# Kernel tuning notes

Measured on AMD Instinct MI355X. Metric: run time of the kernel, lower is better.

## Reference

```python
import jax, jax.numpy as jnp
import numpy as np

WEIGHT = 1.0
BIN_SIZE = 1.0
MAX_MZ = 2000.0
NUM_BINS = int(MAX_MZ / BIN_SIZE)  # 2000
B, N = 8192, 256


def setup_inputs() -> dict:
    key = jax.random.key(0)
    k1, k2, k3, k4, k5 = jax.random.split(key, 5)
    return {
        "pred_mz": jax.random.uniform(k1, (B, N), dtype=jnp.float32),
        "pred_intensity": jax.random.uniform(k2, (B, N), dtype=jnp.float32),
        "target_mz": jax.random.uniform(k3, (B, N), dtype=jnp.float32),
        "target_intensity": jax.random.uniform(k4, (B, N), dtype=jnp.float32),
        "target_mask": jax.random.uniform(k5, (B, N), dtype=jnp.float32),
    }


def _bin_spectrum(mz, intensity):
    # mz is normalized to [0,1]; denormalize and bin. Batched scatter-add:
    # a single 2D indexed add replaces the per-sample scatter_add_ loop.
    bin_idx = jnp.clip((mz * MAX_MZ / BIN_SIZE).astype(jnp.int32), 0, NUM_BINS - 1)  # [B, N]
    bsz = mz.shape[0]
    binned = jnp.zeros((bsz, NUM_BINS), dtype=intensity.dtype)
    return binned.at[jnp.arange(bsz)[:, None], bin_idx].add(intensity)


def reference(pred_mz, pred_intensity, target_mz, target_intensity, target_mask):
    pred_binned = _bin_spectrum(pred_mz, pred_intensity)                    # [B, NUM_BINS]
    target_binned = _bin_spectrum(target_mz, target_intensity * target_mask)
    eps = 1e-8  # matches torch F.cosine_similarity default
    pn = jnp.maximum(jnp.linalg.norm(pred_binned, axis=1), eps)
    tn = jnp.maximum(jnp.linalg.norm(target_binned, axis=1), eps)
    cos = jnp.sum(pred_binned * target_binned, axis=1) / (pn * tn)
    cos = jnp.clip(cos, -1.0, 1.0)
    angle = jnp.arccos(cos)
    loss = jnp.mean(angle / jnp.pi)
    return WEIGHT * loss
```

## Files before the change

### kernel.cpp

```cpp
#include <hip/hip_runtime.h>
#include <math.h>


#define SAL_NUM_BINS 2000
#define SAL_B 8192
#define SAL_N 256

__device__ __forceinline__ float sal_row_angle(
    float* __restrict__ hp, float* __restrict__ hq,
    const float4& pmz, const float4& pin,
    const float4& tmz, const float4& tin,
    bool undo)
{
    const int pb0 = min(max((int)(pmz.x * 2000.0f), 0), SAL_NUM_BINS - 1);
    const int pb1 = min(max((int)(pmz.y * 2000.0f), 0), SAL_NUM_BINS - 1);
    const int pb2 = min(max((int)(pmz.z * 2000.0f), 0), SAL_NUM_BINS - 1);
    const int pb3 = min(max((int)(pmz.w * 2000.0f), 0), SAL_NUM_BINS - 1);
    const int tb0 = min(max((int)(tmz.x * 2000.0f), 0), SAL_NUM_BINS - 1);
    const int tb1 = min(max((int)(tmz.y * 2000.0f), 0), SAL_NUM_BINS - 1);
    const int tb2 = min(max((int)(tmz.z * 2000.0f), 0), SAL_NUM_BINS - 1);
    const int tb3 = min(max((int)(tmz.w * 2000.0f), 0), SAL_NUM_BINS - 1);

    atomicAdd(&hp[pb0], pin.x);
    atomicAdd(&hp[pb1], pin.y);
    atomicAdd(&hp[pb2], pin.z);
    atomicAdd(&hp[pb3], pin.w);
    atomicAdd(&hq[tb0], tin.x);
    atomicAdd(&hq[tb1], tin.y);
    atomicAdd(&hq[tb2], tin.z);
    atomicAdd(&hq[tb3], tin.w);

    float dot = 0.f, p2 = 0.f, t2 = 0.f;
    dot = fmaf(pin.x, hq[pb0], dot);  p2 = fmaf(pin.x, hp[pb0], p2);
    dot = fmaf(pin.y, hq[pb1], dot);  p2 = fmaf(pin.y, hp[pb1], p2);
    dot = fmaf(pin.z, hq[pb2], dot);  p2 = fmaf(pin.z, hp[pb2], p2);
    dot = fmaf(pin.w, hq[pb3], dot);  p2 = fmaf(pin.w, hp[pb3], p2);
    t2  = fmaf(tin.x, hq[tb0], t2);
    t2  = fmaf(tin.y, hq[tb1], t2);
    t2  = fmaf(tin.z, hq[tb2], t2);
    t2  = fmaf(tin.w, hq[tb3], t2);

    if (undo) {
        hp[pb0] = 0.0f; hp[pb1] = 0.0f; hp[pb2] = 0.0f; hp[pb3] = 0.0f;
        hq[tb0] = 0.0f; hq[tb1] = 0.0f; hq[tb2] = 0.0f; hq[tb3] = 0.0f;
    }

    #pragma unroll
    for (int off = 32; off > 0; off >>= 1) {
        dot += __shfl_down(dot, off, 64);
        p2  += __shfl_down(p2,  off, 64);
        t2  += __shfl_down(t2,  off, 64);
    }
    float pn = fmaxf(sqrtf(p2), 1e-8f);
    float tn = fmaxf(sqrtf(t2), 1e-8f);
    float cs = dot / (pn * tn);
    cs = fminf(fmaxf(cs, -1.0f), 1.0f);
    return acosf(cs) * (float)(1.0 / M_PI);
}

__global__ __launch_bounds__(256) void sal_row_kernel(
    const float* __restrict__ pred_mz,
    const float* __restrict__ pred_int,
    const float* __restrict__ targ_mz,
    const float* __restrict__ targ_int,
    const float* __restrict__ targ_mask,
    float* __restrict__ wave_partial)
{
    __shared__ __align__(16) float hist[4][2][SAL_NUM_BINS];
    const int t = threadIdx.x;
    const int w = t >> 6;
    const int l = t & 63;
    const int rowA = blockIdx.x * 8 + w * 2;
    const int baseA = rowA * SAL_N;
    const int baseB = baseA + SAL_N;

    const float4 pmzA = ((const float4*)(pred_mz   + baseA))[l];
    const float4 pinA = ((const float4*)(pred_int  + baseA))[l];
    const float4 tmzA = ((const float4*)(targ_mz   + baseA))[l];
    const float4 ti4A = ((const float4*)(targ_int  + baseA))[l];
    const float4 tm4A = ((const float4*)(targ_mask + baseA))[l];
    const float4 pmzB = ((const float4*)(pred_mz   + baseB))[l];
    const float4 pinB = ((const float4*)(pred_int  + baseB))[l];
    const float4 tmzB = ((const float4*)(targ_mz   + baseB))[l];
    const float4 ti4B = ((const float4*)(targ_int  + baseB))[l];
    const float4 tm4B = ((const float4*)(targ_mask + baseB))[l];

    {
        float4* h4 = (float4*)&hist[w][0][0];
        const float4 z = make_float4(0.f, 0.f, 0.f, 0.f);
        #pragma unroll
        for (int i = 0; i < 16; ++i) {
            int idx = l + i * 64;
            if (idx < (2 * SAL_NUM_BINS) / 4) h4[idx] = z;
        }
    }

    float* hp = &hist[w][0][0];
    float* hq = &hist[w][1][0];

    const float4 tinA = make_float4(ti4A.x * tm4A.x, ti4A.y * tm4A.y,
                                    ti4A.z * tm4A.z, ti4A.w * tm4A.w);
    const float4 tinB = make_float4(ti4B.x * tm4B.x, ti4B.y * tm4B.y,
                                    ti4B.z * tm4B.z, ti4B.w * tm4B.w);

    const float angA = sal_row_angle(hp, hq, pmzA, pinA, tmzA, tinA, true);
    const float angB = sal_row_angle(hp, hq, pmzB, pinB, tmzB, tinB, false);

    if (l == 0) wave_partial[blockIdx.x * 4 + w] = angA + angB;
}

__global__ __launch_bounds__(256) void sal_reduce_kernel(
    const float* __restrict__ wave_partial, float* __restrict__ out)
{
    const int t = threadIdx.x;
    const float4* wp4 = (const float4*)wave_partial;
    float s = 0.0f;
    #pragma unroll
    for (int i = 0; i < 4096 / 4 / 256; ++i) {
        float4 v = wp4[t + i * 256];
        s += (v.x + v.y) + (v.z + v.w);
    }
    #pragma unroll
    for (int off = 32; off > 0; off >>= 1) s += __shfl_down(s, off, 64);
    __shared__ float rbuf[4];
    if ((t & 63) == 0) rbuf[t >> 6] = s;
    __syncthreads();
    if (t == 0) out[0] = ((rbuf[0] + rbuf[1]) + (rbuf[2] + rbuf[3])) * (float)(1.0 / SAL_B);
}

extern "C" void kernel_launch(void* const* d_in, const int* in_sizes, int n_in,
                              void* d_out, int out_size, void* d_ws, size_t ws_size,
                              hipStream_t stream) {
    const float* pred_mz   = (const float*)d_in[0];
    const float* pred_int  = (const float*)d_in[1];
    const float* targ_mz   = (const float*)d_in[2];
    const float* targ_int  = (const float*)d_in[3];
    const float* targ_mask = (const float*)d_in[4];
    float* wave_partial = (float*)d_ws;
    float* out = (float*)d_out;

    sal_row_kernel<<<SAL_B / 8, 256, 0, stream>>>(pred_mz, pred_int, targ_mz,
                                                  targ_int, targ_mask, wave_partial);
    sal_reduce_kernel<<<1, 256, 0, stream>>>(wave_partial, out);
}
```

Measured before the change: 105.3 us.

## Use one shared histogram per single-wave block with sequential target/pred binning

Replaces the 256-thread block, where each wave held two 2000-bin histograms, with 64-thread single-wave blocks that each process two rows. Each block uses one 2000-bin histogram: it bins the target spectrum, reads it back for the dot product and target norm, clears those bins, then reuses the same buffer for the prediction norm. This halves LDS per wave so more waves can be resident per CU, and the grid grows to 4096 blocks. In exchange, each block does more sequential scatter/clear passes, and the reduce kernel now sums 4096 partials.

```diff
diff --git a/kernel.cpp b/kernel.cpp
--- a/kernel.cpp
+++ b/kernel.cpp
@@ -5,108 +5,112 @@
 #define SAL_NUM_BINS 2000
 #define SAL_B 8192
 #define SAL_N 256
+#define SAL_R 2
+#define SAL_GRID (SAL_B / SAL_R)
 
-__device__ __forceinline__ float sal_row_angle(
-    float* __restrict__ hp, float* __restrict__ hq,
-    const float4& pmz, const float4& pin,
-    const float4& tmz, const float4& tin,
-    bool undo)
-{
-    const int pb0 = min(max((int)(pmz.x * 2000.0f), 0), SAL_NUM_BINS - 1);
-    const int pb1 = min(max((int)(pmz.y * 2000.0f), 0), SAL_NUM_BINS - 1);
-    const int pb2 = min(max((int)(pmz.z * 2000.0f), 0), SAL_NUM_BINS - 1);
-    const int pb3 = min(max((int)(pmz.w * 2000.0f), 0), SAL_NUM_BINS - 1);
-    const int tb0 = min(max((int)(tmz.x * 2000.0f), 0), SAL_NUM_BINS - 1);
-    const int tb1 = min(max((int)(tmz.y * 2000.0f), 0), SAL_NUM_BINS - 1);
-    const int tb2 = min(max((int)(tmz.z * 2000.0f), 0), SAL_NUM_BINS - 1);
-    const int tb3 = min(max((int)(tmz.w * 2000.0f), 0), SAL_NUM_BINS - 1);
-
-    atomicAdd(&hp[pb0], pin.x);
-    atomicAdd(&hp[pb1], pin.y);
-    atomicAdd(&hp[pb2], pin.z);
-    atomicAdd(&hp[pb3], pin.w);
-    atomicAdd(&hq[tb0], tin.x);
-    atomicAdd(&hq[tb1], tin.y);
-    atomicAdd(&hq[tb2], tin.z);
-    atomicAdd(&hq[tb3], tin.w);
-
-    float dot = 0.f, p2 = 0.f, t2 = 0.f;
-    dot = fmaf(pin.x, hq[pb0], dot);  p2 = fmaf(pin.x, hp[pb0], p2);
-    dot = fmaf(pin.y, hq[pb1], dot);  p2 = fmaf(pin.y, hp[pb1], p2);
-    dot = fmaf(pin.z, hq[pb2], dot);  p2 = fmaf(pin.z, hp[pb2], p2);
-    dot = fmaf(pin.w, hq[pb3], dot);  p2 = fmaf(pin.w, hp[pb3], p2);
-    t2  = fmaf(tin.x, hq[tb0], t2);
-    t2  = fmaf(tin.y, hq[tb1], t2);
-    t2  = fmaf(tin.z, hq[tb2], t2);
-    t2  = fmaf(tin.w, hq[tb3], t2);
-
-    if (undo) {
-        hp[pb0] = 0.0f; hp[pb1] = 0.0f; hp[pb2] = 0.0f; hp[pb3] = 0.0f;
-        hq[tb0] = 0.0f; hq[tb1] = 0.0f; hq[tb2] = 0.0f; hq[tb3] = 0.0f;
-    }
-
-    #pragma unroll
-    for (int off = 32; off > 0; off >>= 1) {
-        dot += __shfl_down(dot, off, 64);
-        p2  += __shfl_down(p2,  off, 64);
-        t2  += __shfl_down(t2,  off, 64);
-    }
-    float pn = fmaxf(sqrtf(p2), 1e-8f);
-    float tn = fmaxf(sqrtf(t2), 1e-8f);
-    float cs = dot / (pn * tn);
-    cs = fminf(fmaxf(cs, -1.0f), 1.0f);
-    return acosf(cs) * (float)(1.0 / M_PI);
-}
-
-__global__ __launch_bounds__(256) void sal_row_kernel(
+__global__ __launch_bounds__(64, 4) void sal_row_kernel(
     const float* __restrict__ pred_mz,
     const float* __restrict__ pred_int,
     const float* __restrict__ targ_mz,
     const float* __restrict__ targ_int,
     const float* __restrict__ targ_mask,
-    float* __restrict__ wave_partial)
+    float* __restrict__ block_partial)
 {
-    __shared__ __align__(16) float hist[4][2][SAL_NUM_BINS];
-    const int t = threadIdx.x;
-    const int w = t >> 6;
-    const int l = t & 63;
-    const int rowA = blockIdx.x * 8 + w * 2;
-    const int baseA = rowA * SAL_N;
-    const int baseB = baseA + SAL_N;
+    __shared__ __align__(16) float hist[SAL_NUM_BINS];
+    const int l = threadIdx.x;
 
-    const float4 pmzA = ((const float4*)(pred_mz   + baseA))[l];
-    const float4 pinA = ((const float4*)(pred_int  + baseA))[l];
-    const float4 tmzA = ((const float4*)(targ_mz   + baseA))[l];
-    const float4 ti4A = ((const float4*)(targ_int  + baseA))[l];
-    const float4 tm4A = ((const float4*)(targ_mask + baseA))[l];
-    const float4 pmzB = ((const float4*)(pred_mz   + baseB))[l];
-    const float4 pinB = ((const float4*)(pred_int  + baseB))[l];
-    const float4 tmzB = ((const float4*)(targ_mz   + baseB))[l];
-    const float4 ti4B = ((const float4*)(targ_int  + baseB))[l];
-    const float4 tm4B = ((const float4*)(targ_mask + baseB))[l];
+    float4 pmz[SAL_R], pin[SAL_R], tmz[SAL_R], ti4[SAL_R], tm4[SAL_R];
+    #pragma unroll
+    for (int r = 0; r < SAL_R; ++r) {
+        const int base = (blockIdx.x * SAL_R + r) * SAL_N;
+        pmz[r] = ((const float4*)(pred_mz   + base))[l];
+        pin[r] = ((const float4*)(pred_int  + base))[l];
+        tmz[r] = ((const float4*)(targ_mz   + base))[l];
+        ti4[r] = ((const float4*)(targ_int  + base))[l];
+        tm4[r] = ((const float4*)(targ_mask + base))[l];
+    }
 
     {
-        float4* h4 = (float4*)&hist[w][0][0];
+        float4* h4 = (float4*)hist;
         const float4 z = make_float4(0.f, 0.f, 0.f, 0.f);
         #pragma unroll
-        for (int i = 0; i < 16; ++i) {
-            int idx = l + i * 64;
-            if (idx < (2 * SAL_NUM_BINS) / 4) h4[idx] = z;
+        for (int i = 0; i < 8; ++i) {
+            const int idx = l + i * 64;
+            if (idx < SAL_NUM_BINS / 4) h4[idx] = z;
         }
     }
 
-    float* hp = &hist[w][0][0];
-    float* hq = &hist[w][1][0];
+    float dotv[SAL_R], p2v[SAL_R], t2v[SAL_R];
 
-    const float4 tinA = make_float4(ti4A.x * tm4A.x, ti4A.y * tm4A.y,
-                                    ti4A.z * tm4A.z, ti4A.w * tm4A.w);
-    const float4 tinB = make_float4(ti4B.x * tm4B.x, ti4B.y * tm4B.y,
-                                    ti4B.z * tm4B.z, ti4B.w * tm4B.w);
+    #pragma unroll
+    for (int r = 0; r < SAL_R; ++r) {
+        const float4 tin = make_float4(ti4[r].x * tm4[r].x, ti4[r].y * tm4[r].y,
+                                       ti4[r].z * tm4[r].z, ti4[r].w * tm4[r].w);
+        const int pb0 = min(max((int)(pmz[r].x * 2000.0f), 0), SAL_NUM_BINS - 1);
+        const int pb1 = min(max((int)(pmz[r].y * 2000.0f), 0), SAL_NUM_BINS - 1);
+        const int pb2 = min(max((int)(pmz[r].z * 2000.0f), 0), SAL_NUM_BINS - 1);
+        const int pb3 = min(max((int)(pmz[r].w * 2000.0f), 0), SAL_NUM_BINS - 1);
+        const int tb0 = min(max((int)(tmz[r].x * 2000.0f), 0), SAL_NUM_BINS - 1);
+        const int tb1 = min(max((int)(tmz[r].y * 2000.0f), 0), SAL_NUM_BINS - 1);
+        const int tb2 = min(max((int)(tmz[r].z * 2000.0f), 0), SAL_NUM_BINS - 1);
+        const int tb3 = min(max((int)(tmz[r].w * 2000.0f), 0), SAL_NUM_BINS - 1);
 
-    const float angA = sal_row_angle(hp, hq, pmzA, pinA, tmzA, tinA, true);
-    const float angB = sal_row_angle(hp, hq, pmzB, pinB, tmzB, tinB, false);
+        atomicAdd(&hist[tb0], tin.x);
+        atomicAdd(&hist[tb1], tin.y);
+        atomicAdd(&hist[tb2], tin.z);
+        atomicAdd(&hist[tb3], tin.w);
 
-    if (l == 0) wave_partial[blockIdx.x * 4 + w] = angA + angB;
+        float dot = 0.f, p2 = 0.f, t2 = 0.f;
+        dot = fmaf(pin[r].x, hist[pb0], dot);
+        dot = fmaf(pin[r].y, hist[pb1], dot);
+        dot = fmaf(pin[r].z, hist[pb2], dot);
+        dot = fmaf(pin[r].w, hist[pb3], dot);
+        t2  = fmaf(tin.x, hist[tb0], t2);
+        t2  = fmaf(tin.y, hist[tb1], t2);
+        t2  = fmaf(tin.z, hist[tb2], t2);
+        t2  = fmaf(tin.w, hist[tb3], t2);
+
+        hist[tb0] = 0.0f; hist[tb1] = 0.0f; hist[tb2] = 0.0f; hist[tb3] = 0.0f;
+
+        atomicAdd(&hist[pb0], pin[r].x);
+        atomicAdd(&hist[pb1], pin[r].y);
+        atomicAdd(&hist[pb2], pin[r].z);
+        atomicAdd(&hist[pb3], pin[r].w);
+
+        p2 = fmaf(pin[r].x, hist[pb0], p2);
+        p2 = fmaf(pin[r].y, hist[pb1], p2);
+        p2 = fmaf(pin[r].z, hist[pb2], p2);
+        p2 = fmaf(pin[r].w, hist[pb3], p2);
+
+        if (r < SAL_R - 1) {
+            hist[pb0] = 0.0f; hist[pb1] = 0.0f; hist[pb2] = 0.0f; hist[pb3] = 0.0f;
+        }
+
+        dotv[r] = dot; p2v[r] = p2; t2v[r] = t2;
+    }
+
+    #pragma unroll
+    for (int off = 32; off > 0; off >>= 1) {
+        #pragma unroll
+        for (int r = 0; r < SAL_R; ++r) {
+            dotv[r] += __shfl_down(dotv[r], off, 64);
+            p2v[r]  += __shfl_down(p2v[r],  off, 64);
+            t2v[r]  += __shfl_down(t2v[r],  off, 64);
+        }
+    }
+
+    if (l == 0) {
+        float s = 0.f;
+        #pragma unroll
+        for (int r = 0; r < SAL_R; ++r) {
+            const float pn = fmaxf(sqrtf(p2v[r]), 1e-8f);
+            const float tn = fmaxf(sqrtf(t2v[r]), 1e-8f);
+            float cs = dotv[r] / (pn * tn);
+            cs = fminf(fmaxf(cs, -1.0f), 1.0f);
+            s += acosf(cs) * (float)(1.0 / M_PI);
+        }
+        block_partial[blockIdx.x] = s;
+    }
 }
 
 __global__ __launch_bounds__(256) void sal_reduce_kernel(
@@ -116,7 +120,7 @@
     const float4* wp4 = (const float4*)wave_partial;
     float s = 0.0f;
     #pragma unroll
-    for (int i = 0; i < 4096 / 4 / 256; ++i) {
+    for (int i = 0; i < SAL_GRID / 4 / 256; ++i) {
         float4 v = wp4[t + i * 256];
         s += (v.x + v.y) + (v.z + v.w);
     }
@@ -136,10 +140,10 @@
     const float* targ_mz   = (const float*)d_in[2];
     const float* targ_int  = (const float*)d_in[3];
     const float* targ_mask = (const float*)d_in[4];
-    float* wave_partial = (float*)d_ws;
+    float* block_partial = (float*)d_ws;
     float* out = (float*)d_out;
 
-    sal_row_kernel<<<SAL_B / 8, 256, 0, stream>>>(pred_mz, pred_int, targ_mz,
-                                                  targ_int, targ_mask, wave_partial);
-    sal_reduce_kernel<<<1, 256, 0, stream>>>(wave_partial, out);
+    sal_row_kernel<<<SAL_GRID, 64, 0, stream>>>(pred_mz, pred_int, targ_mz,
+                                                targ_int, targ_mask, block_partial);
+    sal_reduce_kernel<<<1, 256, 0, stream>>>(block_partial, out);
 }
```

New measurement: 107.1 us. About the same (+1.7%).
